# Kernel optimization log

Measured on AMD Instinct MI355X. Metric: run time of the kernel, lower is better.

## Reference

```python
import jax, jax.numpy as jnp
import numpy as np

B, E, H, W, N = 2, 16, 160, 288, 12  # batch, embed dim, mask-feat HxW, instances/sample
T = 2  # two frames (mask_feats_1, mask_feats_2)


def setup_inputs() -> dict:
    key = jax.random.key(0)
    k1, k2, k3 = jax.random.split(key, 3)
    return {
        "mask_feats_1": jax.random.normal(k1, (B, E, H, W), jnp.float32),
        "mask_feats_2": jax.random.normal(k2, (B, E, H, W), jnp.float32),
        "gt_final": jax.random.randint(k3, (B, N, T, H, W), 0, 2, jnp.int32),
    }


def _lovasz_hinge(logits, labels):
    # logits, labels: (P,) flattened over (T, H, W); labels in {0,1} float
    signs = 2.0 * labels - 1.0
    errors = 1.0 - logits * signs
    perm = jnp.argsort(-errors)            # descending errors
    errors_sorted = errors[perm]
    gt_sorted = labels[perm]
    gts = gt_sorted.sum()
    inter = gts - jnp.cumsum(gt_sorted)
    union = gts + jnp.cumsum(1.0 - gt_sorted)
    jaccard = 1.0 - inter / union
    jaccard = jnp.concatenate([jaccard[:1], jaccard[1:] - jaccard[:-1]])  # lovasz grad
    return jnp.dot(jax.nn.relu(errors_sorted), jaccard)


def reference(mask_feats_1, mask_feats_2, gt_final):
    # embedding_map: cat on new T dim then permute -> (B, T, H, W, E)
    emb = jnp.stack([mask_feats_1, mask_feats_2], axis=1).transpose(0, 1, 3, 4, 2)
    m = gt_final.astype(jnp.float32)                      # (B, N, T, H, W)
    cnt = m.sum(axis=(2, 3, 4))[..., None]                # (B, N, 1) nonzero pts per instance
    # masked mean of instance embeddings == instance_embeddings.mean(dim=0)
    mean = jnp.einsum('bnthw,bthwe->bne', m, emb) / cnt   # (B, N, E)
    # (emb_map - center)^2 per instance: (B, N, T, H, W, E) -- dominant intermediate
    diff2 = (emb[:, None] - mean[:, :, None, None, None, :]) ** 2
    # unbiased variance over the masked points (torch.var default, dim=0)
    var = jnp.einsum('bnthwe,bnthw->bne', diff2, m) / (cnt - 1.0)
    # probability map: exp(-0.5 * sum(diff^2 * var, -1)) over full T,H,W
    d = jnp.einsum('bnthwe,bne->bnthw', diff2, var)
    logits = 2.0 * jnp.exp(-0.5 * d) - 1.0                # (B, N, T, H, W)
    P = T * H * W
    losses = jax.vmap(jax.vmap(_lovasz_hinge))(logits.reshape(B, N, P), m.reshape(B, N, P))
    total_instances = B * N
    return losses.sum() / total_instances
```

## Files before the change

kernel.cpp:

```cpp
#include <hip/hip_runtime.h>
#include <cstdint>

#define B_ 2
#define E_ 16
#define H_ 160
#define W_ 288
#define N_ 12
#define T_ 2
#define HW_ (H_*W_)
#define P_ (T_*HW_)
#define NINST (B_*N_)
#define NBINS 4096
#define BINSCALE 2048.0f

typedef unsigned long long u64;
typedef unsigned int u32;

__device__ inline float waveReduceSum(float v){
  #pragma unroll
  for(int o=32;o>0;o>>=1) v += __shfl_down(v, o, 64);
  return v;
}

__global__ void k_stats(const float* __restrict__ mf1, const float* __restrict__ mf2,
                        const int* __restrict__ gt,
                        float* __restrict__ sumEmb, float* __restrict__ sumSq,
                        float* __restrict__ cnt){
  int bn = blockIdx.x;
  int b  = bn / N_;
  int base = blockIdx.y * 1024;
  int t = base / HW_;
  int rbase = base - t*HW_;
  const float* ep = (t ? mf2 : mf1) + (size_t)b*E_*HW_;
  const int*   gp = gt + ((size_t)bn*T_ + t)*HW_;

  float s[E_], q[E_]; float c = 0.f;
  #pragma unroll
  for(int e=0;e<E_;e++){ s[e]=0.f; q[e]=0.f; }
  #pragma unroll
  for(int k=0;k<4;k++){
    int r = rbase + k*256 + threadIdx.x;
    float m = (float)gp[r];
    c += m;
    #pragma unroll
    for(int e=0;e<E_;e++){
      float x = ep[(size_t)e*HW_ + r];
      float mx = m*x;
      s[e] += mx;
      q[e] = fmaf(mx, x, q[e]);
    }
  }
  __shared__ float red[2*E_+1];
  if(threadIdx.x < 2*E_+1) red[threadIdx.x] = 0.f;
  __syncthreads();
  int lane = threadIdx.x & 63;
  #pragma unroll
  for(int e=0;e<E_;e++){
    float r1 = waveReduceSum(s[e]);
    if(lane==0) atomicAdd(&red[e], r1);
    float r2 = waveReduceSum(q[e]);
    if(lane==0) atomicAdd(&red[E_+e], r2);
  }
  { float r = waveReduceSum(c); if(lane==0) atomicAdd(&red[2*E_], r); }
  __syncthreads();
  if(threadIdx.x < E_)            atomicAdd(&sumEmb[bn*E_ + threadIdx.x], red[threadIdx.x]);
  else if(threadIdx.x < 2*E_)     atomicAdd(&sumSq [bn*E_ + threadIdx.x - E_], red[threadIdx.x]);
  else if(threadIdx.x == 2*E_)    atomicAdd(&cnt[bn], red[2*E_]);
}

__global__ void k_fin(const float* __restrict__ sumEmb, const float* __restrict__ sumSq,
                      const float* __restrict__ cnt,
                      float* __restrict__ mean, float* __restrict__ var){
  int i = threadIdx.x;
  float c  = cnt[i>>4];
  float mu = sumEmb[i] / c;
  mean[i] = mu;
  var[i]  = (sumSq[i] - c*mu*mu) / (c - 1.0f);
}

__global__ __launch_bounds__(256) void k_err(const float* __restrict__ mf1,
                                             const float* __restrict__ mf2,
                                             const int* __restrict__ gt,
                                             const float* __restrict__ mean,
                                             const float* __restrict__ var,
                                             u64* __restrict__ hist,
                                             float* __restrict__ esum){
  __shared__ u32   hcl[NBINS];
  __shared__ float hes[NBINS];
  int bn = blockIdx.x;
  int b  = bn / N_;
  for(int i=threadIdx.x; i<NBINS; i+=256){ hcl[i]=0u; hes[i]=0.f; }

  float mn[E_], sv[E_];
  #pragma unroll
  for(int e=0;e<E_;e++){ mn[e]=mean[bn*E_+e]; sv[e]=var[bn*E_+e]; }

  int pbase = blockIdx.y * 3072;
  int t = pbase / HW_;
  int rbase = pbase - t*HW_;
  const float* ep = (t ? mf2 : mf1) + (size_t)b*E_*HW_;
  const int*   gp = gt + (size_t)bn*P_ + pbase;
  __syncthreads();

  #pragma unroll
  for(int it=0; it<12; ++it){
    int r = rbase + it*256 + threadIdx.x;
    float d = 0.f;
    #pragma unroll
    for(int e=0;e<E_;e++){
      float df = ep[(size_t)e*HW_ + r] - mn[e];
      d = fmaf(df*df, sv[e], d);
    }
    float logits = 2.f*__expf(-0.5f*d) - 1.f;
    int   mi = gp[it*256 + threadIdx.x];
    float ev = fmaxf(1.f - logits*(2.f*(float)mi - 1.f), 0.f);
    int bin = min(NBINS-1, (int)(ev * BINSCALE));
    atomicAdd(&hcl[bin], 0x10000u | (u32)mi);
    atomicAdd(&hes[bin], ev);
  }
  __syncthreads();

  u64*   hp = hist + (size_t)bn*NBINS;
  float* sp = esum + (size_t)bn*NBINS;
  for(int i=threadIdx.x; i<NBINS; i+=256){
    u32 v = hcl[i];
    if(v){
      atomicAdd(&hp[i], ((u64)(v>>16)<<32) | (u64)(v & 0xffffu));
      atomicAdd(&sp[i], hes[i]);
    }
  }
}

__global__ __launch_bounds__(256) void k_bins(const u64* __restrict__ hist,
                                              const float* __restrict__ esum,
                                              const float* __restrict__ cnt,
                                              float* __restrict__ out){
  const int PT = NBINS/256;
  int bn = blockIdx.x;
  const u64*   h  = hist + (size_t)bn*NBINS;
  const float* es = esum + (size_t)bn*NBINS;
  int tid = threadIdx.x, lane = tid & 63, wave = tid >> 6;

  u64 loc[PT]; u64 s = 0;
  #pragma unroll
  for(int k=0;k<PT;k++){
    loc[k] = h[NBINS-1 - (tid*PT + k)];
    s += loc[k];
  }
  u64 sc = s;
  #pragma unroll
  for(int off=1;off<64;off<<=1){ u64 v = __shfl_up(sc, off, 64); if(lane>=off) sc += v; }
  __shared__ u64 wsum[4], wbase[4];
  if(lane==63) wsum[wave] = sc;
  __syncthreads();
  if(tid==0){
    u64 run = 0;
    #pragma unroll
    for(int w=0;w<4;w++){ wbase[w] = run; run += wsum[w]; }
  }
  __syncthreads();
  u64 excl = wbase[wave] + (sc - s);

  float G = cnt[bn];
  float lsum = 0.f;
  #pragma unroll
  for(int k=0;k<PT;k++){
    u64 lv = loc[k];
    u32 cb = (u32)(lv>>32), lb = (u32)(lv & 0xffffffffu);
    if(cb){
      float i0 = (float)(u32)(excl>>32);
      float c0 = (float)(u32)(excl & 0xffffffffu);
      float c1 = c0 + (float)lb;
      float jend   = 1.f - (G - c1)/(G + i0 + (float)cb - c1);
      float jstart = 1.f - (G - c0)/(G + i0 - c0);
      lsum += (es[NBINS-1 - (tid*PT + k)] / (float)cb) * (jend - jstart);
    }
    excl += lv;
  }

  __shared__ float rs[4];
  float tot = waveReduceSum(lsum);
  if(lane==0) rs[wave] = tot;
  __syncthreads();
  if(tid==0) atomicAdd(out, (rs[0]+rs[1]+rs[2]+rs[3]) * (1.0f/(float)NINST));
}

extern "C" void kernel_launch(void* const* d_in, const int* in_sizes, int n_in,
                              void* d_out, int out_size, void* d_ws, size_t ws_size,
                              hipStream_t stream){
  const float* mf1 = (const float*)d_in[0];
  const float* mf2 = (const float*)d_in[1];
  const int*   gt  = (const int*)d_in[2];
  float* out = (float*)d_out;

  float* sumEmb = (float*)d_ws;
  float* cnt    = sumEmb + 384;
  float* mean   = cnt + 24;
  float* var    = mean + 384;
  float* sumSq  = var + 384;
  u64*   hist   = (u64*)((char*)d_ws + 8192);
  float* esum   = (float*)((char*)hist + (size_t)NINST*NBINS*8);
  size_t zbytes = 8192 + (size_t)NINST*NBINS*8 + (size_t)NINST*NBINS*4;

  hipMemsetAsync(d_ws, 0, zbytes, stream);
  hipMemsetAsync(d_out, 0, sizeof(float), stream);

  k_stats<<<dim3(NINST, P_/1024), 256, 0, stream>>>(mf1, mf2, gt, sumEmb, sumSq, cnt);
  k_fin<<<1, 384, 0, stream>>>(sumEmb, sumSq, cnt, mean, var);
  k_err<<<dim3(NINST, P_/3072), 256, 0, stream>>>(mf1, mf2, gt, mean, var, hist, esum);
  k_bins<<<NINST, 256, 0, stream>>>(hist, esum, cnt, out);
}
```

Measured before the change: 140.7 us.

## Share embedding loads across instances, shrink histogram, drop error-sum bins and k_fin

Restructures the stats and error kernels so one block covers all 12 instances of a batch sample. Each embedding vector is loaded once and reused across instances instead of being reloaded per instance. The mean/variance finalize kernel is folded into k_err. The histogram shrinks from 4096 to 512 bins, and the per-bin error sum is replaced by the bin midpoint, which removes the float shared/global atomics and the esum buffer. The coarser binning plus midpoint approximation adds quantization error to the Lovasz loss and could exceed tolerance.

```diff
diff --git a/kernel.cpp b/kernel.cpp
--- a/kernel.cpp
+++ b/kernel.cpp
@@ -10,8 +10,8 @@
 #define HW_ (H_*W_)
 #define P_ (T_*HW_)
 #define NINST (B_*N_)
-#define NBINS 4096
-#define BINSCALE 2048.0f
+#define NBINS 512
+#define BINSCALE 256.0f
 
 typedef unsigned long long u64;
 typedef unsigned int u32;
@@ -22,25 +22,30 @@
   return v;
 }
 
-__global__ void k_stats(const float* __restrict__ mf1, const float* __restrict__ mf2,
-                        const int* __restrict__ gt,
-                        float* __restrict__ sumEmb, float* __restrict__ sumSq,
-                        float* __restrict__ cnt){
-  int bn = blockIdx.x;
-  int b  = bn / N_;
-  int base = blockIdx.y * 1024;
-  int t = base / HW_;
-  int rbase = base - t*HW_;
+__global__ __launch_bounds__(768) void k_stats(const float* __restrict__ mf1,
+                                               const float* __restrict__ mf2,
+                                               const int* __restrict__ gt,
+                                               float* __restrict__ sumEmb,
+                                               float* __restrict__ sumSq,
+                                               float* __restrict__ cnt){
+  int b    = blockIdx.x;
+  int w    = threadIdx.x >> 6;
+  int lane = threadIdx.x & 63;
+  int bn   = b*N_ + w;
+  int pbase = blockIdx.y * 512;
+  int t = pbase / HW_;
+  int rbase = pbase - t*HW_;
   const float* ep = (t ? mf2 : mf1) + (size_t)b*E_*HW_;
-  const int*   gp = gt + ((size_t)bn*T_ + t)*HW_;
+  const int*   gp = gt + (size_t)bn*P_ + pbase;
 
   float s[E_], q[E_]; float c = 0.f;
   #pragma unroll
   for(int e=0;e<E_;e++){ s[e]=0.f; q[e]=0.f; }
   #pragma unroll
-  for(int k=0;k<4;k++){
-    int r = rbase + k*256 + threadIdx.x;
-    float m = (float)gp[r];
+  for(int it=0; it<8; ++it){
+    int idx = it*64 + lane;
+    int r = rbase + idx;
+    float m = (float)gp[idx];
     c += m;
     #pragma unroll
     for(int e=0;e<E_;e++){
@@ -50,95 +55,81 @@
       q[e] = fmaf(mx, x, q[e]);
     }
   }
-  __shared__ float red[2*E_+1];
-  if(threadIdx.x < 2*E_+1) red[threadIdx.x] = 0.f;
-  __syncthreads();
-  int lane = threadIdx.x & 63;
   #pragma unroll
   for(int e=0;e<E_;e++){
     float r1 = waveReduceSum(s[e]);
-    if(lane==0) atomicAdd(&red[e], r1);
     float r2 = waveReduceSum(q[e]);
-    if(lane==0) atomicAdd(&red[E_+e], r2);
-  }
-  { float r = waveReduceSum(c); if(lane==0) atomicAdd(&red[2*E_], r); }
-  __syncthreads();
-  if(threadIdx.x < E_)            atomicAdd(&sumEmb[bn*E_ + threadIdx.x], red[threadIdx.x]);
-  else if(threadIdx.x < 2*E_)     atomicAdd(&sumSq [bn*E_ + threadIdx.x - E_], red[threadIdx.x]);
-  else if(threadIdx.x == 2*E_)    atomicAdd(&cnt[bn], red[2*E_]);
-}
-
-__global__ void k_fin(const float* __restrict__ sumEmb, const float* __restrict__ sumSq,
-                      const float* __restrict__ cnt,
-                      float* __restrict__ mean, float* __restrict__ var){
-  int i = threadIdx.x;
-  float c  = cnt[i>>4];
-  float mu = sumEmb[i] / c;
-  mean[i] = mu;
-  var[i]  = (sumSq[i] - c*mu*mu) / (c - 1.0f);
-}
-
-__global__ __launch_bounds__(256) void k_err(const float* __restrict__ mf1,
+    if(lane==0){
+      atomicAdd(&sumEmb[bn*E_ + e], r1);
+      atomicAdd(&sumSq [bn*E_ + e], r2);
+    }
+  }
+  float rc = waveReduceSum(c);
+  if(lane==0) atomicAdd(&cnt[bn], rc);
+}
+
+__global__ __launch_bounds__(512) void k_err(const float* __restrict__ mf1,
                                              const float* __restrict__ mf2,
                                              const int* __restrict__ gt,
-                                             const float* __restrict__ mean,
-                                             const float* __restrict__ var,
-                                             u64* __restrict__ hist,
-                                             float* __restrict__ esum){
-  __shared__ u32   hcl[NBINS];
-  __shared__ float hes[NBINS];
-  int bn = blockIdx.x;
-  int b  = bn / N_;
-  for(int i=threadIdx.x; i<NBINS; i+=256){ hcl[i]=0u; hes[i]=0.f; }
-
-  float mn[E_], sv[E_];
-  #pragma unroll
-  for(int e=0;e<E_;e++){ mn[e]=mean[bn*E_+e]; sv[e]=var[bn*E_+e]; }
-
-  int pbase = blockIdx.y * 3072;
-  int t = pbase / HW_;
-  int rbase = pbase - t*HW_;
+                                             const float* __restrict__ sumEmb,
+                                             const float* __restrict__ sumSq,
+                                             const float* __restrict__ cnt,
+                                             u64* __restrict__ hist){
+  __shared__ float smn[N_*E_], ssv[N_*E_];
+  __shared__ u32 hcl[N_*NBINS];
+  int b = blockIdx.x;
+  int tid = threadIdx.x;
+  if(tid < N_*E_){
+    float c  = cnt[b*N_ + (tid>>4)];
+    float mu = sumEmb[b*N_*E_ + tid] / c;
+    smn[tid] = mu;
+    ssv[tid] = (sumSq[b*N_*E_ + tid] - c*mu*mu) / (c - 1.0f);
+  }
+  #pragma unroll
+  for(int k=0;k<N_*NBINS/512;k++) hcl[k*512 + tid] = 0u;
+
+  int p = blockIdx.y*512 + tid;
+  int t = p / HW_;
+  int r = p - t*HW_;
   const float* ep = (t ? mf2 : mf1) + (size_t)b*E_*HW_;
-  const int*   gp = gt + (size_t)bn*P_ + pbase;
-  __syncthreads();
-
-  #pragma unroll
-  for(int it=0; it<12; ++it){
-    int r = rbase + it*256 + threadIdx.x;
+  float x[E_];
+  #pragma unroll
+  for(int e=0;e<E_;e++) x[e] = ep[(size_t)e*HW_ + r];
+  __syncthreads();
+
+  #pragma unroll
+  for(int n=0;n<N_;n++){
+    int bn = b*N_ + n;
     float d = 0.f;
     #pragma unroll
     for(int e=0;e<E_;e++){
-      float df = ep[(size_t)e*HW_ + r] - mn[e];
-      d = fmaf(df*df, sv[e], d);
+      float df = x[e] - smn[n*E_+e];
+      d = fmaf(df*df, ssv[n*E_+e], d);
     }
     float logits = 2.f*__expf(-0.5f*d) - 1.f;
-    int   mi = gp[it*256 + threadIdx.x];
+    int   mi = gt[(size_t)bn*P_ + p];
     float ev = fmaxf(1.f - logits*(2.f*(float)mi - 1.f), 0.f);
     int bin = min(NBINS-1, (int)(ev * BINSCALE));
-    atomicAdd(&hcl[bin], 0x10000u | (u32)mi);
-    atomicAdd(&hes[bin], ev);
-  }
-  __syncthreads();
-
-  u64*   hp = hist + (size_t)bn*NBINS;
-  float* sp = esum + (size_t)bn*NBINS;
-  for(int i=threadIdx.x; i<NBINS; i+=256){
+    atomicAdd(&hcl[n*NBINS + bin], 0x10000u | (u32)mi);
+  }
+  __syncthreads();
+
+  for(int i=tid; i<N_*NBINS; i+=512){
     u32 v = hcl[i];
     if(v){
-      atomicAdd(&hp[i], ((u64)(v>>16)<<32) | (u64)(v & 0xffffu));
-      atomicAdd(&sp[i], hes[i]);
+      int n = i / NBINS, bin = i - n*NBINS;
+      atomicAdd(&hist[(size_t)(b*N_+n)*NBINS + bin],
+                ((u64)(v>>16)<<32) | (u64)(v & 0xffffu));
     }
   }
 }
 
 __global__ __launch_bounds__(256) void k_bins(const u64* __restrict__ hist,
-                                              const float* __restrict__ esum,
                                               const float* __restrict__ cnt,
                                               float* __restrict__ out){
   const int PT = NBINS/256;
   int bn = blockIdx.x;
-  const u64*   h  = hist + (size_t)bn*NBINS;
-  const float* es = esum + (size_t)bn*NBINS;
+  const u64* h = hist + (size_t)bn*NBINS;
   int tid = threadIdx.x, lane = tid & 63, wave = tid >> 6;
 
   u64 loc[PT]; u64 s = 0;
@@ -168,12 +159,14 @@
     u64 lv = loc[k];
     u32 cb = (u32)(lv>>32), lb = (u32)(lv & 0xffffffffu);
     if(cb){
+      int bin = NBINS-1 - (tid*PT + k);
+      float mid = ((float)bin + 0.5f) * (1.0f/BINSCALE);
       float i0 = (float)(u32)(excl>>32);
       float c0 = (float)(u32)(excl & 0xffffffffu);
       float c1 = c0 + (float)lb;
       float jend   = 1.f - (G - c1)/(G + i0 + (float)cb - c1);
       float jstart = 1.f - (G - c0)/(G + i0 - c0);
-      lsum += (es[NBINS-1 - (tid*PT + k)] / (float)cb) * (jend - jstart);
+      lsum += mid * (jend - jstart);
     }
     excl += lv;
   }
@@ -195,18 +188,14 @@
 
   float* sumEmb = (float*)d_ws;
   float* cnt    = sumEmb + 384;
-  float* mean   = cnt + 24;
-  float* var    = mean + 384;
-  float* sumSq  = var + 384;
+  float* sumSq  = cnt + 24;
   u64*   hist   = (u64*)((char*)d_ws + 8192);
-  float* esum   = (float*)((char*)hist + (size_t)NINST*NBINS*8);
-  size_t zbytes = 8192 + (size_t)NINST*NBINS*8 + (size_t)NINST*NBINS*4;
+  size_t zbytes = 8192 + (size_t)NINST*NBINS*sizeof(u64);
 
   hipMemsetAsync(d_ws, 0, zbytes, stream);
   hipMemsetAsync(d_out, 0, sizeof(float), stream);
 
-  k_stats<<<dim3(NINST, P_/1024), 256, 0, stream>>>(mf1, mf2, gt, sumEmb, sumSq, cnt);
-  k_fin<<<1, 384, 0, stream>>>(sumEmb, sumSq, cnt, mean, var);
-  k_err<<<dim3(NINST, P_/3072), 256, 0, stream>>>(mf1, mf2, gt, mean, var, hist, esum);
-  k_bins<<<NINST, 256, 0, stream>>>(hist, esum, cnt, out);
-}
+  k_stats<<<dim3(B_, P_/512), 768, 0, stream>>>(mf1, mf2, gt, sumEmb, sumSq, cnt);
+  k_err<<<dim3(B_, P_/512), 512, 0, stream>>>(mf1, mf2, gt, sumEmb, sumSq, cnt, hist);
+  k_bins<<<NINST, 256, 0, stream>>>(hist, cnt, out);
+}
```

Result: slower. 187.5 us (+33.3%).
